# Optimization experiments

Hardware: AMD Instinct MI355X
Metric: run time of the kernel (lower is better)

Reference implementation:

```python
import jax, jax.numpy as jnp
import numpy as np

N_USER = 100000
N_ITEM = 100000
E = 300000
S = 128   # memory / GRU hidden dim (in_feats_s)
T = 128   # time encode dim (in_feats_t)
DE = 128  # edge feature dim
M = 2 * S + T + DE  # GRU input dim (in_feats_m) = 512


def setup_inputs() -> dict:
    key = jax.random.key(0)
    ks = jax.random.split(key, 10)
    si = jax.random.normal(ks[0], (N_USER, S), jnp.float32)
    sj = jax.random.normal(ks[1], (N_ITEM, S), jnp.float32)
    t = jax.random.uniform(ks[2], (E,), jnp.float32)
    e = jax.random.normal(ks[3], (E, DE), jnp.float32)
    src = jax.random.randint(ks[4], (E,), 0, N_USER, jnp.int32)
    dst = jax.random.randint(ks[5], (E,), 0, N_ITEM, jnp.int32)
    # GRU params (torch layout: weight_ih [3H, M], weight_hh [3H, H])
    Wi = jax.random.normal(ks[6], (3 * S, M), jnp.float32) * 0.05
    Wh = jax.random.normal(ks[7], (3 * S, S), jnp.float32) * 0.05
    bi = jax.random.normal(ks[8], (3 * S,), jnp.float32) * 0.05
    bh = jax.random.normal(ks[9], (3 * S,), jnp.float32) * 0.05
    # TimeEncode non-trainable params (phase is zeros, folded out)
    basis_freq = jnp.asarray(1.0 / 10.0 ** np.linspace(0, 9, T), jnp.float32)
    return {"si": si, "sj": sj, "t": t, "e": e, "src": src, "dst": dst,
            "Wi": Wi, "Wh": Wh, "bi": bi, "bh": bh, "basis_freq": basis_freq}


def _last_message(mail, idx, n):
    # DGL last_reduce: message of the highest-edge-id incoming edge per node; zeros if none.
    eid = jnp.arange(mail.shape[0], dtype=jnp.int32)
    last = jax.ops.segment_max(eid, idx, num_segments=n)  # int32 min for empty segments
    has = last >= 0
    safe = jnp.where(has, last, 0)
    return jnp.where(has[:, None], mail[safe], jnp.zeros((), mail.dtype))


def _gru_step(x, h, Wi, Wh, bi, bh):
    gi = x @ Wi.T + bi
    gh = h @ Wh.T + bh
    gir, giz, gin = jnp.split(gi, 3, axis=1)
    ghr, ghz, ghn = jnp.split(gh, 3, axis=1)
    r = jax.nn.sigmoid(gir + ghr)
    z = jax.nn.sigmoid(giz + ghz)
    n = jnp.tanh(gin + r * ghn)
    return (1.0 - z) * n + z * h


def reference(si, sj, t, e, src, dst, Wi, Wh, bi, bh, basis_freq):
    # sinusoidal time encoding (phase = 0)
    te = jnp.cos(t[:, None] * basis_freq[None, :])  # [E, T]
    si_e = si[src]  # [E, S] gather user memory per edge
    sj_e = sj[dst]  # [E, S] gather item memory per edge
    # forward graph g (user->item): mail = [src_mem, dst_mem, time, e], reduce to items
    mail_f = jnp.concatenate([si_e, sj_e, te, e], axis=1)  # [E, M]
    # reverse graph g_r (item->user): src=item, dst=user
    mail_r = jnp.concatenate([sj_e, si_e, te, e], axis=1)  # [E, M]
    mj = _last_message(mail_f, dst, N_ITEM)  # [N_ITEM, M]
    mi = _last_message(mail_r, src, N_USER)  # [N_USER, M]
    si_new = _gru_step(mi, si, Wi, Wh, bi, bh)
    sj_new = _gru_step(mj, sj, Wi, Wh, bi, bh)
    return (si_new, sj_new)
```

## Files before the change

### kernel.cpp

```cpp
#include <hip/hip_runtime.h>
#include <hip/hip_bf16.h>

#define N_USER 100000
#define N_ITEM 100000
#define NE     300000
#define S      128

typedef __attribute__((ext_vector_type(8))) short short8;
typedef __attribute__((ext_vector_type(4))) float floatx4;
typedef unsigned long long ull;

static __device__ __forceinline__ short f2bf(float x) {
  union { float f; unsigned u; } a; a.f = x;
  unsigned r = a.u + 0x7FFFu + ((a.u >> 16) & 1u);
  return (short)(r >> 16);
}

__global__ void last_edge_kernel(const int* __restrict__ src, const int* __restrict__ dst,
                                 int* __restrict__ last_u, int* __restrict__ last_v) {
  int i = blockIdx.x * 256 + threadIdx.x;
  if (i < NE) {
    atomicMax(&last_u[src[i]], i);
    atomicMax(&last_v[dst[i]], i);
  }
}

__global__ void wpack_kernel(const float* __restrict__ Wi, const float* __restrict__ Wh,
                             short* __restrict__ Wp) {
  int id = blockIdx.x * 256 + threadIdx.x;
  int ks   = id / 1536;
  int rem  = id - ks * 1536;
  int lane = rem & 63;
  int col  = (rem >> 6) * 16 + (lane & 15);
  int kof  = (lane >> 4) * 8;
  const float* p = (ks < 16) ? (Wi + (size_t)col * 512 + ks * 32 + kof)
                             : (Wh + (size_t)col * 128 + (ks - 16) * 32 + kof);
  floatx4 a = *(const floatx4*)p;
  floatx4 b = *(const floatx4*)(p + 4);
  short8 v;
  v[0] = f2bf(a[0]); v[1] = f2bf(a[1]); v[2] = f2bf(a[2]); v[3] = f2bf(a[3]);
  v[4] = f2bf(b[0]); v[5] = f2bf(b[1]); v[6] = f2bf(b[2]); v[7] = f2bf(b[3]);
  *(short8*)(Wp + (size_t)id * 8) = v;
}

__global__ __launch_bounds__(256, 2)
void fused_gru_kernel(const float* __restrict__ si, const float* __restrict__ sj,
                      const float* __restrict__ tt, const float* __restrict__ ef,
                      const int* __restrict__ src, const int* __restrict__ dst,
                      const float* __restrict__ bi, const float* __restrict__ bh,
                      const float* __restrict__ basis,
                      const int* __restrict__ last_u, const int* __restrict__ last_v,
                      const short* __restrict__ Wp, const float* __restrict__ zpage,
                      float* __restrict__ out) {
  __shared__ short As[10 * 4 * 64 * 8];
  __shared__ ull   Atab[64][4];
  __shared__ float Ttv[64];
  __shared__ float Tsc[64];

  const int tid  = threadIdx.x;
  const int lane = tid & 63;
  const int w    = tid >> 6;
  const int row0 = blockIdx.x * 64;

  if (tid < 64) {
    int g = row0 + tid;
    bool isU = g < N_USER;
    int node = isU ? g : g - N_USER;
    const float* own = (isU ? si : sj) + (size_t)node * S;
    int l = isU ? last_u[node] : last_v[node];
    const float *a0, *a1, *a3; float tv, sc;
    if (l >= 0) {
      int o = isU ? dst[l] : src[l];
      a0 = (isU ? sj : si) + (size_t)o * S;
      a1 = own;
      a3 = ef + (size_t)l * S;
      tv = tt[l]; sc = 1.f;
    } else {
      a0 = zpage; a1 = zpage; a3 = zpage; tv = 0.f; sc = 0.f;
    }
    Atab[tid][0] = (ull)a0; Atab[tid][1] = (ull)a1;
    Atab[tid][2] = (ull)a3; Atab[tid][3] = (ull)own;
    Ttv[tid] = tv; Tsc[tid] = sc;
  }
  __syncthreads();

  floatx4 acc[32];
  #pragma unroll
  for (int i = 0; i < 32; ++i) acc[i] = (floatx4){0.f, 0.f, 0.f, 0.f};

  const int r = tid >> 2;

  #pragma unroll 1
  for (int ph = 0; ph < 2; ++ph) {
    if (ph) __syncthreads();

    #pragma unroll 2
    for (int p = 0; p < 10; ++p) {
      int K0  = ph * 320 + p * 32 + (tid & 3) * 8;
      int seg = K0 >> 7;
      int off = K0 & 127;
      short8 v;
      if (seg == 2) {
        float tv = Ttv[r], sc = Tsc[r];
        floatx4 b0 = *(const floatx4*)(basis + off);
        floatx4 b1 = *(const floatx4*)(basis + off + 4);
        v[0] = f2bf(__cosf(tv * b0[0]) * sc); v[1] = f2bf(__cosf(tv * b0[1]) * sc);
        v[2] = f2bf(__cosf(tv * b0[2]) * sc); v[3] = f2bf(__cosf(tv * b0[3]) * sc);
        v[4] = f2bf(__cosf(tv * b1[0]) * sc); v[5] = f2bf(__cosf(tv * b1[1]) * sc);
        v[6] = f2bf(__cosf(tv * b1[2]) * sc); v[7] = f2bf(__cosf(tv * b1[3]) * sc);
      } else {
        int slot = (seg >= 3) ? seg - 1 : seg;
        const float* p0 = (const float*)Atab[r][slot] + off;
        floatx4 a = *(const floatx4*)p0;
        floatx4 b = *(const floatx4*)(p0 + 4);
        v[0] = f2bf(a[0]); v[1] = f2bf(a[1]); v[2] = f2bf(a[2]); v[3] = f2bf(a[3]);
        v[4] = f2bf(b[0]); v[5] = f2bf(b[1]); v[6] = f2bf(b[2]); v[7] = f2bf(b[3]);
      }
      int ksr   = (K0 >> 5) - ph * 10;
      int laneF = (r & 15) + 16 * ((K0 >> 3) & 3);
      *(short8*)&As[(((ksr * 4) + (r >> 4)) * 64 + laneF) * 8] = v;
    }
    __syncthreads();

    short8 bc[6], bn[6], ac[4], an[4];
    #pragma unroll
    for (int i = 0; i < 6; ++i)
      bc[i] = *(const short8*)(Wp + (size_t)(((ph * 10) * 24 + (w + 4 * i)) * 64 + lane) * 8);
    #pragma unroll
    for (int rf = 0; rf < 4; ++rf)
      ac[rf] = *(const short8*)&As[((0 * 4 + rf) * 64 + lane) * 8];

    #pragma unroll 1
    for (int ksr = 0; ksr < 10; ++ksr) {
      if (ksr < 9) {
        #pragma unroll
        for (int i = 0; i < 6; ++i)
          bn[i] = *(const short8*)(Wp + (size_t)(((ph * 10 + ksr + 1) * 24 + (w + 4 * i)) * 64 + lane) * 8);
        #pragma unroll
        for (int rf = 0; rf < 4; ++rf)
          an[rf] = *(const short8*)&As[(((ksr + 1) * 4 + rf) * 64 + lane) * 8];
      }
      #pragma unroll
      for (int i = 0; i < 4; ++i)
        #pragma unroll
        for (int rf = 0; rf < 4; ++rf)
          acc[i * 4 + rf] = __builtin_amdgcn_mfma_f32_16x16x32_bf16(ac[rf], bc[i], acc[i * 4 + rf], 0, 0, 0);
      if (ph == 1 && ksr >= 6) {
        #pragma unroll
        for (int i = 4; i < 6; ++i)
          #pragma unroll
          for (int rf = 0; rf < 4; ++rf)
            acc[24 + (i - 4) * 4 + rf] = __builtin_amdgcn_mfma_f32_16x16x32_bf16(ac[rf], bc[i], acc[24 + (i - 4) * 4 + rf], 0, 0, 0);
      } else {
        #pragma unroll
        for (int i = 4; i < 6; ++i)
          #pragma unroll
          for (int rf = 0; rf < 4; ++rf)
            acc[i * 4 + rf] = __builtin_amdgcn_mfma_f32_16x16x32_bf16(ac[rf], bc[i], acc[i * 4 + rf], 0, 0, 0);
      }
      #pragma unroll
      for (int i = 0; i < 6; ++i) bc[i] = bn[i];
      #pragma unroll
      for (int rf = 0; rf < 4; ++rf) ac[rf] = an[rf];
    }
  }

  const int colb = lane & 15;
  const int krow = (lane >> 4) * 4;
  #pragma unroll
  for (int h = 0; h < 2; ++h) {
    int c = (w + 4 * h) * 16 + colb;
    float br  = bi[c]       + bh[c];
    float bz  = bi[128 + c] + bh[128 + c];
    float bni = bi[256 + c];
    float bnh = bh[256 + c];
    #pragma unroll
    for (int rf = 0; rf < 4; ++rf) {
      #pragma unroll
      for (int k = 0; k < 4; ++k) {
        int row = rf * 16 + krow + k;
        int g = row0 + row;
        const float* hp = (g < N_USER) ? (si + (size_t)g * S)
                                       : (sj + (size_t)(g - N_USER) * S);
        float rpre = acc[h * 4 + rf][k]        + br;
        float zpre = acc[(2 + h) * 4 + rf][k]  + bz;
        float gin  = acc[(4 + h) * 4 + rf][k]  + bni;
        float ghn  = acc[24 + h * 4 + rf][k]   + bnh;
        float rg = 1.f / (1.f + __expf(-rpre));
        float zg = 1.f / (1.f + __expf(-zpre));
        float x  = gin + rg * ghn;
        float nn = 1.f - 2.f / (__expf(2.f * x) + 1.f);
        out[(size_t)g * S + c] = (1.f - zg) * nn + zg * hp[c];
      }
    }
  }
}

extern "C" void kernel_launch(void* const* d_in, const int* in_sizes, int n_in,
                              void* d_out, int out_size, void* d_ws, size_t ws_size,
                              hipStream_t stream) {
  const float* si    = (const float*)d_in[0];
  const float* sj    = (const float*)d_in[1];
  const float* tt    = (const float*)d_in[2];
  const float* ef    = (const float*)d_in[3];
  const int*   src   = (const int*)d_in[4];
  const int*   dst   = (const int*)d_in[5];
  const float* Wi    = (const float*)d_in[6];
  const float* Wh    = (const float*)d_in[7];
  const float* bi    = (const float*)d_in[8];
  const float* bh    = (const float*)d_in[9];
  const float* basis = (const float*)d_in[10];

  int*   last_u = (int*)d_ws;
  int*   last_v = last_u + N_USER;
  float* zpage  = (float*)((char*)d_ws + 800000);
  short* Wp     = (short*)((char*)d_ws + (1 << 20));

  hipMemsetAsync(last_u, 0xFF, (size_t)(N_USER + N_ITEM) * sizeof(int), stream);
  hipMemsetAsync(zpage, 0, 128 * sizeof(float), stream);
  last_edge_kernel<<<(NE + 255) / 256, 256, 0, stream>>>(src, dst, last_u, last_v);
  wpack_kernel<<<120, 256, 0, stream>>>(Wi, Wh, Wp);
  fused_gru_kernel<<<(N_USER + N_ITEM) / 64, 256, 0, stream>>>(
      si, sj, tt, ef, src, dst, bi, bh, basis, last_u, last_v, Wp, zpage, (float*)d_out);
}
```

Measured before the change: 512.7 us.

## Halve GRU row tile, single-phase K loop, batched gathers, fuse prep kernels

The fused GRU kernel now handles 32 rows per block instead of 64. It stages the whole 640-wide K dimension into shared memory in one pass, issuing all ten gathered loads per thread before converting them, and runs a single fully unrolled 20-step MFMA loop with occupancy raised to 3 blocks per SM. The weight pack, zero-page init and last-edge atomics are merged into one prep kernel to save launches and a memset. Smaller tiles double how often each block reloads the packed weights, in exchange for more blocks in flight and more memory-level parallelism on the random gathers.

```diff
diff --git a/kernel.cpp b/kernel.cpp
--- a/kernel.cpp
+++ b/kernel.cpp
@@ -16,34 +16,39 @@
   return (short)(r >> 16);
 }
 
-__global__ void last_edge_kernel(const int* __restrict__ src, const int* __restrict__ dst,
-                                 int* __restrict__ last_u, int* __restrict__ last_v) {
-  int i = blockIdx.x * 256 + threadIdx.x;
-  if (i < NE) {
-    atomicMax(&last_u[src[i]], i);
-    atomicMax(&last_v[dst[i]], i);
-  }
-}
-
-__global__ void wpack_kernel(const float* __restrict__ Wi, const float* __restrict__ Wh,
-                             short* __restrict__ Wp) {
-  int id = blockIdx.x * 256 + threadIdx.x;
-  int ks   = id / 1536;
-  int rem  = id - ks * 1536;
-  int lane = rem & 63;
-  int col  = (rem >> 6) * 16 + (lane & 15);
-  int kof  = (lane >> 4) * 8;
-  const float* p = (ks < 16) ? (Wi + (size_t)col * 512 + ks * 32 + kof)
-                             : (Wh + (size_t)col * 128 + (ks - 16) * 32 + kof);
-  floatx4 a = *(const floatx4*)p;
-  floatx4 b = *(const floatx4*)(p + 4);
-  short8 v;
-  v[0] = f2bf(a[0]); v[1] = f2bf(a[1]); v[2] = f2bf(a[2]); v[3] = f2bf(a[3]);
-  v[4] = f2bf(b[0]); v[5] = f2bf(b[1]); v[6] = f2bf(b[2]); v[7] = f2bf(b[3]);
-  *(short8*)(Wp + (size_t)id * 8) = v;
-}
-
-__global__ __launch_bounds__(256, 2)
+__global__ void prep_kernel(const int* __restrict__ src, const int* __restrict__ dst,
+                            int* __restrict__ last_u, int* __restrict__ last_v,
+                            const float* __restrict__ Wi, const float* __restrict__ Wh,
+                            short* __restrict__ Wp, float* __restrict__ zpage) {
+  int b = blockIdx.x;
+  int tid = threadIdx.x;
+  if (b < 120) {
+    int id   = b * 256 + tid;
+    int ks   = id / 1536;
+    int rem  = id - ks * 1536;
+    int lane = rem & 63;
+    int col  = (rem >> 6) * 16 + (lane & 15);
+    int kof  = (lane >> 4) * 8;
+    const float* p = (ks < 16) ? (Wi + (size_t)col * 512 + ks * 32 + kof)
+                               : (Wh + (size_t)col * 128 + (ks - 16) * 32 + kof);
+    floatx4 a = *(const floatx4*)p;
+    floatx4 c = *(const floatx4*)(p + 4);
+    short8 v;
+    v[0] = f2bf(a[0]); v[1] = f2bf(a[1]); v[2] = f2bf(a[2]); v[3] = f2bf(a[3]);
+    v[4] = f2bf(c[0]); v[5] = f2bf(c[1]); v[6] = f2bf(c[2]); v[7] = f2bf(c[3]);
+    *(short8*)(Wp + (size_t)id * 8) = v;
+  } else if (b == 120) {
+    if (tid < 128) zpage[tid] = 0.f;
+  } else {
+    int i = (b - 121) * 256 + tid;
+    if (i < NE) {
+      atomicMax(&last_u[src[i]], i);
+      atomicMax(&last_v[dst[i]], i);
+    }
+  }
+}
+
+__global__ __launch_bounds__(256, 3)
 void fused_gru_kernel(const float* __restrict__ si, const float* __restrict__ sj,
                       const float* __restrict__ tt, const float* __restrict__ ef,
                       const int* __restrict__ src, const int* __restrict__ dst,
@@ -52,17 +57,17 @@
                       const int* __restrict__ last_u, const int* __restrict__ last_v,
                       const short* __restrict__ Wp, const float* __restrict__ zpage,
                       float* __restrict__ out) {
-  __shared__ short As[10 * 4 * 64 * 8];
-  __shared__ ull   Atab[64][4];
-  __shared__ float Ttv[64];
-  __shared__ float Tsc[64];
+  __shared__ short As[20 * 2 * 64 * 8];
+  __shared__ ull   Atab[32][5];
+  __shared__ float Ttv[32];
+  __shared__ float Tsc[32];
 
   const int tid  = threadIdx.x;
   const int lane = tid & 63;
   const int w    = tid >> 6;
-  const int row0 = blockIdx.x * 64;
-
-  if (tid < 64) {
+  const int row0 = blockIdx.x * 32;
+
+  if (tid < 32) {
     int g = row0 + tid;
     bool isU = g < N_USER;
     int node = isU ? g : g - N_USER;
@@ -78,91 +83,92 @@
     } else {
       a0 = zpage; a1 = zpage; a3 = zpage; tv = 0.f; sc = 0.f;
     }
-    Atab[tid][0] = (ull)a0; Atab[tid][1] = (ull)a1;
-    Atab[tid][2] = (ull)a3; Atab[tid][3] = (ull)own;
+    Atab[tid][0] = (ull)a0; Atab[tid][1] = (ull)a1; Atab[tid][2] = (ull)basis;
+    Atab[tid][3] = (ull)a3; Atab[tid][4] = (ull)own;
     Ttv[tid] = tv; Tsc[tid] = sc;
   }
   __syncthreads();
 
-  floatx4 acc[32];
-  #pragma unroll
-  for (int i = 0; i < 32; ++i) acc[i] = (floatx4){0.f, 0.f, 0.f, 0.f};
-
-  const int r = tid >> 2;
-
-  #pragma unroll 1
-  for (int ph = 0; ph < 2; ++ph) {
-    if (ph) __syncthreads();
-
-    #pragma unroll 2
-    for (int p = 0; p < 10; ++p) {
-      int K0  = ph * 320 + p * 32 + (tid & 3) * 8;
-      int seg = K0 >> 7;
-      int off = K0 & 127;
+  {
+    const int srf = w & 1;
+    const int row = srf * 16 + (lane & 15);
+    const int kco = (lane >> 4) * 8;
+    const int ksb = w >> 1;
+    const float tv = Ttv[row], sc = Tsc[row];
+
+    floatx4 va[10], vb[10];
+    #pragma unroll
+    for (int it = 0; it < 10; ++it) {
+      const int seg = it >> 1;
+      const int ks  = it * 2 + ksb;
+      const int off = ((ks & 3) * 32) + kco;
+      const float* p = (const float*)Atab[row][seg] + off;
+      va[it] = *(const floatx4*)p;
+      vb[it] = *(const floatx4*)(p + 4);
+    }
+    #pragma unroll
+    for (int it = 0; it < 10; ++it) {
       short8 v;
-      if (seg == 2) {
-        float tv = Ttv[r], sc = Tsc[r];
-        floatx4 b0 = *(const floatx4*)(basis + off);
-        floatx4 b1 = *(const floatx4*)(basis + off + 4);
-        v[0] = f2bf(__cosf(tv * b0[0]) * sc); v[1] = f2bf(__cosf(tv * b0[1]) * sc);
-        v[2] = f2bf(__cosf(tv * b0[2]) * sc); v[3] = f2bf(__cosf(tv * b0[3]) * sc);
-        v[4] = f2bf(__cosf(tv * b1[0]) * sc); v[5] = f2bf(__cosf(tv * b1[1]) * sc);
-        v[6] = f2bf(__cosf(tv * b1[2]) * sc); v[7] = f2bf(__cosf(tv * b1[3]) * sc);
+      if (it == 4 || it == 5) {
+        v[0] = f2bf(__cosf(tv * va[it][0]) * sc); v[1] = f2bf(__cosf(tv * va[it][1]) * sc);
+        v[2] = f2bf(__cosf(tv * va[it][2]) * sc); v[3] = f2bf(__cosf(tv * va[it][3]) * sc);
+        v[4] = f2bf(__cosf(tv * vb[it][0]) * sc); v[5] = f2bf(__cosf(tv * vb[it][1]) * sc);
+        v[6] = f2bf(__cosf(tv * vb[it][2]) * sc); v[7] = f2bf(__cosf(tv * vb[it][3]) * sc);
       } else {
-        int slot = (seg >= 3) ? seg - 1 : seg;
-        const float* p0 = (const float*)Atab[r][slot] + off;
-        floatx4 a = *(const floatx4*)p0;
-        floatx4 b = *(const floatx4*)(p0 + 4);
-        v[0] = f2bf(a[0]); v[1] = f2bf(a[1]); v[2] = f2bf(a[2]); v[3] = f2bf(a[3]);
-        v[4] = f2bf(b[0]); v[5] = f2bf(b[1]); v[6] = f2bf(b[2]); v[7] = f2bf(b[3]);
+        v[0] = f2bf(va[it][0]); v[1] = f2bf(va[it][1]);
+        v[2] = f2bf(va[it][2]); v[3] = f2bf(va[it][3]);
+        v[4] = f2bf(vb[it][0]); v[5] = f2bf(vb[it][1]);
+        v[6] = f2bf(vb[it][2]); v[7] = f2bf(vb[it][3]);
       }
-      int ksr   = (K0 >> 5) - ph * 10;
-      int laneF = (r & 15) + 16 * ((K0 >> 3) & 3);
-      *(short8*)&As[(((ksr * 4) + (r >> 4)) * 64 + laneF) * 8] = v;
-    }
-    __syncthreads();
-
-    short8 bc[6], bn[6], ac[4], an[4];
-    #pragma unroll
-    for (int i = 0; i < 6; ++i)
-      bc[i] = *(const short8*)(Wp + (size_t)(((ph * 10) * 24 + (w + 4 * i)) * 64 + lane) * 8);
-    #pragma unroll
-    for (int rf = 0; rf < 4; ++rf)
-      ac[rf] = *(const short8*)&As[((0 * 4 + rf) * 64 + lane) * 8];
-
-    #pragma unroll 1
-    for (int ksr = 0; ksr < 10; ++ksr) {
-      if (ksr < 9) {
+      *(short8*)&As[(it * 256 + tid) * 8] = v;
+    }
+  }
+  __syncthreads();
+
+  floatx4 acc[16];
+  #pragma unroll
+  for (int i = 0; i < 16; ++i) acc[i] = (floatx4){0.f, 0.f, 0.f, 0.f};
+
+  short8 aC[2], bC[6], aN[2], bN[6];
+  #pragma unroll
+  for (int r2 = 0; r2 < 2; ++r2)
+    aC[r2] = *(const short8*)&As[((0 * 2 + r2) * 64 + lane) * 8];
+  #pragma unroll
+  for (int i = 0; i < 6; ++i)
+    bC[i] = *(const short8*)(Wp + (size_t)(((0 * 24) + w + 4 * i) * 64 + lane) * 8);
+
+  #pragma unroll
+  for (int ksr = 0; ksr < 20; ++ksr) {
+    if (ksr < 19) {
+      #pragma unroll
+      for (int r2 = 0; r2 < 2; ++r2)
+        aN[r2] = *(const short8*)&As[(((ksr + 1) * 2 + r2) * 64 + lane) * 8];
+      #pragma unroll
+      for (int i = 0; i < 6; ++i)
+        bN[i] = *(const short8*)(Wp + (size_t)(((ksr + 1) * 24 + w + 4 * i) * 64 + lane) * 8);
+    }
+    #pragma unroll
+    for (int i = 0; i < 4; ++i)
+      #pragma unroll
+      for (int r2 = 0; r2 < 2; ++r2)
+        acc[i * 2 + r2] = __builtin_amdgcn_mfma_f32_16x16x32_bf16(aC[r2], bC[i], acc[i * 2 + r2], 0, 0, 0);
+    if (ksr >= 16) {
+      #pragma unroll
+      for (int i = 4; i < 6; ++i)
         #pragma unroll
-        for (int i = 0; i < 6; ++i)
-          bn[i] = *(const short8*)(Wp + (size_t)(((ph * 10 + ksr + 1) * 24 + (w + 4 * i)) * 64 + lane) * 8);
+        for (int r2 = 0; r2 < 2; ++r2)
+          acc[12 + (i - 4) * 2 + r2] = __builtin_amdgcn_mfma_f32_16x16x32_bf16(aC[r2], bC[i], acc[12 + (i - 4) * 2 + r2], 0, 0, 0);
+    } else {
+      #pragma unroll
+      for (int i = 4; i < 6; ++i)
         #pragma unroll
-        for (int rf = 0; rf < 4; ++rf)
-          an[rf] = *(const short8*)&As[(((ksr + 1) * 4 + rf) * 64 + lane) * 8];
-      }
-      #pragma unroll
-      for (int i = 0; i < 4; ++i)
-        #pragma unroll
-        for (int rf = 0; rf < 4; ++rf)
-          acc[i * 4 + rf] = __builtin_amdgcn_mfma_f32_16x16x32_bf16(ac[rf], bc[i], acc[i * 4 + rf], 0, 0, 0);
-      if (ph == 1 && ksr >= 6) {
-        #pragma unroll
-        for (int i = 4; i < 6; ++i)
-          #pragma unroll
-          for (int rf = 0; rf < 4; ++rf)
-            acc[24 + (i - 4) * 4 + rf] = __builtin_amdgcn_mfma_f32_16x16x32_bf16(ac[rf], bc[i], acc[24 + (i - 4) * 4 + rf], 0, 0, 0);
-      } else {
-        #pragma unroll
-        for (int i = 4; i < 6; ++i)
-          #pragma unroll
-          for (int rf = 0; rf < 4; ++rf)
-            acc[i * 4 + rf] = __builtin_amdgcn_mfma_f32_16x16x32_bf16(ac[rf], bc[i], acc[i * 4 + rf], 0, 0, 0);
-      }
-      #pragma unroll
-      for (int i = 0; i < 6; ++i) bc[i] = bn[i];
-      #pragma unroll
-      for (int rf = 0; rf < 4; ++rf) ac[rf] = an[rf];
-    }
+        for (int r2 = 0; r2 < 2; ++r2)
+          acc[i * 2 + r2] = __builtin_amdgcn_mfma_f32_16x16x32_bf16(aC[r2], bC[i], acc[i * 2 + r2], 0, 0, 0);
+    }
+    #pragma unroll
+    for (int r2 = 0; r2 < 2; ++r2) aC[r2] = aN[r2];
+    #pragma unroll
+    for (int i = 0; i < 6; ++i) bC[i] = bN[i];
   }
 
   const int colb = lane & 15;
@@ -175,17 +181,17 @@
     float bni = bi[256 + c];
     float bnh = bh[256 + c];
     #pragma unroll
-    for (int rf = 0; rf < 4; ++rf) {
+    for (int r2 = 0; r2 < 2; ++r2) {
       #pragma unroll
       for (int k = 0; k < 4; ++k) {
-        int row = rf * 16 + krow + k;
+        int row = r2 * 16 + krow + k;
         int g = row0 + row;
         const float* hp = (g < N_USER) ? (si + (size_t)g * S)
                                        : (sj + (size_t)(g - N_USER) * S);
-        float rpre = acc[h * 4 + rf][k]        + br;
-        float zpre = acc[(2 + h) * 4 + rf][k]  + bz;
-        float gin  = acc[(4 + h) * 4 + rf][k]  + bni;
-        float ghn  = acc[24 + h * 4 + rf][k]   + bnh;
+        float rpre = acc[h * 2 + r2][k]       + br;
+        float zpre = acc[(2 + h) * 2 + r2][k] + bz;
+        float gin  = acc[(4 + h) * 2 + r2][k] + bni;
+        float ghn  = acc[12 + h * 2 + r2][k]  + bnh;
         float rg = 1.f / (1.f + __expf(-rpre));
         float zg = 1.f / (1.f + __expf(-zpre));
         float x  = gin + rg * ghn;
@@ -217,9 +223,8 @@
   short* Wp     = (short*)((char*)d_ws + (1 << 20));
 
   hipMemsetAsync(last_u, 0xFF, (size_t)(N_USER + N_ITEM) * sizeof(int), stream);
-  hipMemsetAsync(zpage, 0, 128 * sizeof(float), stream);
-  last_edge_kernel<<<(NE + 255) / 256, 256, 0, stream>>>(src, dst, last_u, last_v);
-  wpack_kernel<<<120, 256, 0, stream>>>(Wi, Wh, Wp);
-  fused_gru_kernel<<<(N_USER + N_ITEM) / 64, 256, 0, stream>>>(
+  prep_kernel<<<121 + (NE + 255) / 256, 256, 0, stream>>>(src, dst, last_u, last_v,
+                                                          Wi, Wh, Wp, zpage);
+  fused_gru_kernel<<<(N_USER + N_ITEM) / 32, 256, 0, stream>>>(
       si, sj, tt, ef, src, dst, bi, bh, basis, last_u, last_v, Wp, zpage, (float*)d_out);
 }
```

Result: faster. 496.4 us (-3.2%).
